# Kernel optimization log

Hardware: AMD Instinct MI355X
Metric: run time of the kernel (lower is better)

Reference implementation:

```python
import jax, jax.numpy as jnp
import numpy as np
import itertools as it

K = 10          # delay taps
SKIP = 2        # stride between taps
TRANSIENTS = 100
P = 3           # monomial degree

# monomial index table: all degree-P combinations_with_replacement of the K linear features
_MONOM_IDX = jnp.asarray(list(it.combinations_with_replacement(range(K), P)), dtype=jnp.int32)  # [nlin_dim, P]


def setup_inputs() -> dict:
    key = jax.random.key(0)
    X = jax.random.normal(key, (8, 4, 4096), dtype=jnp.float32)  # [batch, row, n_steps]
    return {"X": X}


def reference(X):
    # X: [b, r, n]; n_dim = 1 after the original unsqueeze(3)
    b, r, n = X.shape
    pad = (K - 1) * SKIP
    # zero-padded delay embedding replaces the roll loop:
    # lin_features[b,r,i,j] = X[b,r, i - (K-1-j)*SKIP], zero for negative time
    Xpad = jnp.pad(X, ((0, 0), (0, 0), (pad, 0)))           # [b, r, n+pad]
    idx = jnp.arange(n)[:, None] + jnp.arange(K)[None, :] * SKIP  # [n, K]
    lin_features = Xpad[:, :, idx]                          # [b, r, n, K]
    # monomial (degree-P) features: gather then product over the small P axis
    nlin_features = jnp.prod(lin_features[..., _MONOM_IDX], axis=-1)  # [b, r, n, nlin_dim]
    tot = jnp.concatenate([lin_features, nlin_features], axis=3)[:, :, TRANSIENTS:, :]
    ones = jnp.ones(tot.shape[:3] + (1,), dtype=tot.dtype)  # bias column
    return jnp.concatenate([ones, tot], axis=3)             # [b, r, n-TRANSIENTS, 1+K+nlin_dim]
```

## Files before the change

kernel.cpp:

```cpp
#include <hip/hip_runtime.h>

#define KTAPS 10
#define SKIP  2
#define TRANS 100
#define PAD   ((KTAPS - 1) * SKIP)
#define NFEAT 231
#define NIN   4096
#define NT    (NIN - TRANS)
#define NROWS 32
#define TT    40
#define NTILES ((NT + TT - 1) / TT)

__global__ __launch_bounds__(64) void nvar_kernel(const float* __restrict__ X,
                                                  float* __restrict__ out) {
    __shared__ __align__(16) float feat[TT * NFEAT];

    const int tile = blockIdx.x;
    const int row  = blockIdx.y;
    const int t0   = tile * TT;
    const int tcount = min(TT, NT - t0);

    const int tl = threadIdx.x;
    const float* xrow = X + (size_t)row * NIN;

    if (tl < TT) {
        int tg = t0 + tl;
        if (tg >= NT) tg = NT - 1;

        float tap[KTAPS];
#pragma unroll
        for (int k = 0; k < KTAPS; ++k)
            tap[k] = xrow[tg + (TRANS - PAD) + 2 * k];

        float* frow = feat + tl * NFEAT;
        frow[0] = 1.0f;
#pragma unroll
        for (int k = 0; k < KTAPS; ++k)
            frow[1 + k] = tap[k];

        int fb = 1 + KTAPS;
#pragma unroll
        for (int i = 0; i < KTAPS; ++i) {
#pragma unroll
            for (int j = i; j < KTAPS; ++j) {
                const float pij = tap[i] * tap[j];
#pragma unroll
                for (int l = j; l < KTAPS; ++l)
                    frow[fb + (l - j)] = pij * tap[l];
                fb += KTAPS - j;
            }
        }
    }

    __syncthreads();

    const int total4 = (tcount * NFEAT) >> 2;
    float4* __restrict__ o4 =
        reinterpret_cast<float4*>(out + ((size_t)row * NT + t0) * NFEAT);
    const float4* s4 = reinterpret_cast<const float4*>(feat);
#pragma unroll 4
    for (int i = threadIdx.x; i < total4; i += 64)
        o4[i] = s4[i];
}

extern "C" void kernel_launch(void* const* d_in, const int* in_sizes, int n_in,
                              void* d_out, int out_size, void* d_ws, size_t ws_size,
                              hipStream_t stream) {
    const float* X = (const float*)d_in[0];
    float* out = (float*)d_out;
    dim3 grid(NTILES, NROWS);
    nvar_kernel<<<grid, 64, 0, stream>>>(X, out);
}
```

Before: 125.1 us.

## Map one thread per output feature and drop shared-memory staging

Restructures the kernel so each thread owns a feature column and loops over a chunk of 128 time steps, computing its monomial from three strided reads of X and writing directly to global memory. This removes the shared-memory staging, the barrier, and the serial per-time-step compute done by only 40 of 64 threads. Stores become scalar, coalesced across adjacent features within a row, instead of float4 copies. Redundant input loads, which are cache-resident, and the 25 idle lanes per block are the cost.

```diff
diff --git a/kernel.cpp b/kernel.cpp
--- a/kernel.cpp
+++ b/kernel.cpp
@@ -8,59 +8,53 @@
 #define NIN   4096
 #define NT    (NIN - TRANS)
 #define NROWS 32
-#define TT    40
-#define NTILES ((NT + TT - 1) / TT)
+#define CHUNK 128
+#define NCHUNK ((NT + CHUNK - 1) / CHUNK)
 
-__global__ __launch_bounds__(64) void nvar_kernel(const float* __restrict__ X,
-                                                  float* __restrict__ out) {
-    __shared__ __align__(16) float feat[TT * NFEAT];
+__global__ __launch_bounds__(256) void nvar_kernel(const float* __restrict__ X,
+                                                   float* __restrict__ out) {
+    const int f   = threadIdx.x;
+    const int row = blockIdx.y;
+    const int t0  = blockIdx.x * CHUNK;
+    const int tcount = min(CHUNK, NT - t0);
+    if (f >= NFEAT) return;
 
-    const int tile = blockIdx.x;
-    const int row  = blockIdx.y;
-    const int t0   = tile * TT;
-    const int tcount = min(TT, NT - t0);
+    const bool is_one = (f == 0);
+    const bool is_lin = (f >= 1 && f <= KTAPS);
+    int aoff = 0, boff = 0, coff = 0;
+    if (is_lin) {
+        aoff = 2 * (f - 1);
+    } else if (f > KTAPS) {
+        int rem = f - (KTAPS + 1);
+        for (int i = 0; i < KTAPS; ++i)
+            for (int j = i; j < KTAPS; ++j) {
+                const int c = KTAPS - j;
+                if (rem >= 0 && rem < c) { aoff = 2 * i; boff = 2 * j; coff = 2 * (j + rem); }
+                rem -= c;
+            }
+    }
 
-    const int tl = threadIdx.x;
-    const float* xrow = X + (size_t)row * NIN;
+    const float* __restrict__ xp = X + (size_t)row * NIN + t0 + (TRANS - PAD);
+    float* __restrict__ op = out + ((size_t)row * NT + t0) * NFEAT + f;
 
-    if (tl < TT) {
-        int tg = t0 + tl;
-        if (tg >= NT) tg = NT - 1;
-
-        float tap[KTAPS];
+    int t = 0;
+    for (; t + 16 <= tcount; t += 16) {
 #pragma unroll
-        for (int k = 0; k < KTAPS; ++k)
-            tap[k] = xrow[tg + (TRANS - PAD) + 2 * k];
-
-        float* frow = feat + tl * NFEAT;
-        frow[0] = 1.0f;
-#pragma unroll
-        for (int k = 0; k < KTAPS; ++k)
-            frow[1 + k] = tap[k];
-
-        int fb = 1 + KTAPS;
-#pragma unroll
-        for (int i = 0; i < KTAPS; ++i) {
-#pragma unroll
-            for (int j = i; j < KTAPS; ++j) {
-                const float pij = tap[i] * tap[j];
-#pragma unroll
-                for (int l = j; l < KTAPS; ++l)
-                    frow[fb + (l - j)] = pij * tap[l];
-                fb += KTAPS - j;
-            }
+        for (int u = 0; u < 16; ++u) {
+            const float va = xp[aoff + t + u];
+            const float vb = xp[boff + t + u];
+            const float vc = xp[coff + t + u];
+            const float v = is_one ? 1.0f : (is_lin ? va : va * vb * vc);
+            op[(t + u) * NFEAT] = v;
         }
     }
-
-    __syncthreads();
-
-    const int total4 = (tcount * NFEAT) >> 2;
-    float4* __restrict__ o4 =
-        reinterpret_cast<float4*>(out + ((size_t)row * NT + t0) * NFEAT);
-    const float4* s4 = reinterpret_cast<const float4*>(feat);
-#pragma unroll 4
-    for (int i = threadIdx.x; i < total4; i += 64)
-        o4[i] = s4[i];
+    for (; t < tcount; ++t) {
+        const float va = xp[aoff + t];
+        const float vb = xp[boff + t];
+        const float vc = xp[coff + t];
+        const float v = is_one ? 1.0f : (is_lin ? va : va * vb * vc);
+        op[t * NFEAT] = v;
+    }
 }
 
 extern "C" void kernel_launch(void* const* d_in, const int* in_sizes, int n_in,
@@ -68,6 +62,6 @@
                               hipStream_t stream) {
     const float* X = (const float*)d_in[0];
     float* out = (float*)d_out;
-    dim3 grid(NTILES, NROWS);
-    nvar_kernel<<<grid, 64, 0, stream>>>(X, out);
+    dim3 grid(NCHUNK, NROWS);
+    nvar_kernel<<<grid, 256, 0, stream>>>(X, out);
 }
```

Measured after the change: 127.9 us. 2.3% more time.
